# Kernel tuning notes

Measured on AMD Instinct MI355X. Metric: run time of the kernel, lower is better.

## Reference

```python
import jax, jax.numpy as jnp
import numpy as np

B, N, D = 2048, 65536, 128  # batch queries, max_engrams, spike_dim


def setup_inputs() -> dict:
    key = jax.random.key(0)
    k1, k2, k3, k4 = jax.random.split(key, 4)
    sensor_spikes = jax.random.normal(k1, (B, D), dtype=jnp.float32)
    # crystallize_skill stores sign(pattern), so keys/values are +-1 vectors
    sensor_keys = jnp.sign(jax.random.normal(k2, (N, D), dtype=jnp.float32))
    action_values = jnp.sign(jax.random.normal(k3, (N, D), dtype=jnp.float32))
    is_active = jax.random.bernoulli(k4, 0.5, (N,))
    return {
        "sensor_spikes": sensor_spikes,
        "sensor_keys": sensor_keys,
        "action_values": action_values,
        "is_active": is_active,
    }


def reference(sensor_spikes, sensor_keys, action_values, is_active):
    # similarity = x @ keys.T  -> [B, N]
    sim = jnp.einsum("bd,nd->bn", sensor_spikes.astype(jnp.float32), sensor_keys)
    # masked_fill_(~is_active, -inf)
    sim = jnp.where(is_active[None, :], sim, -jnp.inf)
    best_match_idx = jnp.argmax(sim, axis=-1)          # [B]
    confidence = jnp.max(sim, axis=-1)                 # [B] == sim[b, best_idx[b]]
    retrieved = action_values[best_match_idx]          # [B, D]
    return retrieved, confidence, best_match_idx
```

## Files before the change

### kernel.cpp

```cpp
#include <hip/hip_runtime.h>
#include <stdint.h>

typedef __attribute__((ext_vector_type(8))) short short8;
typedef __attribute__((ext_vector_type(4))) float f32x4;

#define NEG_INF (-__builtin_inff())

#define B_ROWS 2048
#define N_KEYS 65536
#define DIM    128


__device__ __forceinline__ unsigned short f2bf(float f) {
  unsigned u = __float_as_uint(f);
  u = (u + 0x7FFFu + ((u >> 16) & 1u)) >> 16;
  return (unsigned short)u;
}


__global__ __launch_bounds__(256) void convert_x_kernel(
    const float* __restrict__ x, short8* __restrict__ xi) {
  int t = blockIdx.x * 256 + threadIdx.x;
  int tile = t >> 11, loc = t & 2047;
  int rl = ((loc >> 8) << 4) + (loc & 15);
  int c = (loc >> 4) & 15;
  const float* src = x + (size_t)(tile * 128 + rl) * DIM + c * 8;
  f32x4 v0 = *(const f32x4*)(src);
  f32x4 v1 = *(const f32x4*)(src + 4);
  short8 o;
  o[0] = (short)f2bf(v0[0]); o[1] = (short)f2bf(v0[1]);
  o[2] = (short)f2bf(v0[2]); o[3] = (short)f2bf(v0[3]);
  o[4] = (short)f2bf(v1[0]); o[5] = (short)f2bf(v1[1]);
  o[6] = (short)f2bf(v1[2]); o[7] = (short)f2bf(v1[3]);
  xi[t] = o;
}

__global__ __launch_bounds__(256, 2) void sim3_kernel(
    const short8* __restrict__ xi, const float* __restrict__ keys,
    const int* __restrict__ act, float* __restrict__ cmax) {
  __shared__ short8 Bs[2048];
  const int tid = threadIdx.x;
  const int w = tid >> 6, l = tid & 63;
  const int ntile = blockIdx.x;

  const float* kb = keys + (size_t)ntile * (128 * DIM);
#pragma unroll
  for (int it = 0; it < 8; ++it) {
    int li = it * 256 + tid;
    int rl = ((li >> 8) << 4) + (li & 15);
    int c = (li >> 4) & 15;
    const float* src = kb + rl * DIM + c * 8;
    f32x4 v0 = *(const f32x4*)(src);
    f32x4 v1 = *(const f32x4*)(src + 4);
    int a = act[ntile * 128 + rl];
    short8 o;
    o[0] = (short)f2bf(v0[0]); o[1] = (short)f2bf(v0[1]);
    o[2] = (short)f2bf(v0[2]); o[3] = (short)f2bf(v0[3]);
    o[4] = (short)f2bf(v1[0]); o[5] = (short)f2bf(v1[1]);
    o[6] = (short)f2bf(v1[2]); o[7] = (short)f2bf(v1[3]);
    if (!a) o = short8{0, 0, 0, 0, 0, 0, 0, 0};
    Bs[li] = o;
  }
  __syncthreads();

  const int wr = w >> 1, wc = w & 1;
  const int lg = l >> 4, lr = l & 15;

  short8 bfv[4][4];
#pragma unroll
  for (int ni = 0; ni < 4; ni++)
#pragma unroll
    for (int kk = 0; kk < 4; kk++)
      bfv[ni][kk] = Bs[(wc * 4 + ni) * 256 + kk * 64 + l];

  const int chunk = ntile * 2 + wc;
  const short8* ag0 = xi + (wr * 4) * 256 + l;

  for (int bt = 0; bt < 16; ++bt) {
    short8 af[4][4];
#pragma unroll
    for (int mi = 0; mi < 4; mi++)
#pragma unroll
      for (int kk = 0; kk < 4; kk++)
        af[mi][kk] = ag0[(size_t)bt * 2048 + mi * 256 + kk * 64];

    f32x4 acc[4][4];
#pragma unroll
    for (int mi = 0; mi < 4; mi++)
#pragma unroll
      for (int ni = 0; ni < 4; ni++) acc[mi][ni] = f32x4{0.f, 0.f, 0.f, 0.f};

#pragma unroll
    for (int kk = 0; kk < 4; kk++)
#pragma unroll
      for (int mi = 0; mi < 4; mi++)
#pragma unroll
        for (int ni = 0; ni < 4; ni++)
          acc[mi][ni] = __builtin_amdgcn_mfma_f32_16x16x32_bf16(
              af[mi][kk], bfv[ni][kk], acc[mi][ni], 0, 0, 0);

#pragma unroll
    for (int mi = 0; mi < 4; mi++) {
      float rm[4];
#pragma unroll
      for (int r = 0; r < 4; r++)
        rm[r] = fmaxf(fmaxf(acc[mi][0][r], acc[mi][1][r]),
                      fmaxf(acc[mi][2][r], acc[mi][3][r]));
#pragma unroll
      for (int r = 0; r < 4; r++) {
        float v = rm[r];
        v = fmaxf(v, __shfl_xor(v, 1));
        v = fmaxf(v, __shfl_xor(v, 2));
        v = fmaxf(v, __shfl_xor(v, 4));
        v = fmaxf(v, __shfl_xor(v, 8));
        rm[r] = v;
      }
      if (lr == 0) {
        int row = bt * 128 + wr * 64 + mi * 16 + lg * 4;
#pragma unroll
        for (int r = 0; r < 4; r++)
          cmax[(size_t)(row + r) * 1024 + chunk] = rm[r];
      }
    }
  }
}

__global__ __launch_bounds__(256) void finalize_kernel(
    const float* __restrict__ x, const float* __restrict__ keys,
    const float* __restrict__ vals, const int* __restrict__ act,
    const float* __restrict__ cmax, float* __restrict__ out) {
  __shared__ float xr[128];
  __shared__ float wred[4];
  __shared__ int cand[96];
  __shared__ int ncand;
  __shared__ int bestn_s;
  __shared__ float skeys[64 * 129];
  const int b = blockIdx.x, tid = threadIdx.x;
  if (tid < 128) xr[tid] = x[(size_t)b * 128 + tid];
  if (tid == 0) ncand = 0;
  __syncthreads();

  const float* cm = cmax + (size_t)b * 1024;
  float c0 = cm[tid], c1 = cm[tid + 256], c2 = cm[tid + 512], c3 = cm[tid + 768];
  float lm = fmaxf(fmaxf(c0, c1), fmaxf(c2, c3));
#pragma unroll
  for (int s = 1; s < 64; s <<= 1) lm = fmaxf(lm, __shfl_xor(lm, s));
  if ((tid & 63) == 0) wred[tid >> 6] = lm;
  __syncthreads();
  float M = fmaxf(fmaxf(wred[0], wred[1]), fmaxf(wred[2], wred[3]));
  float thr = M - 0.75f;

  if (c0 > thr) { int p = atomicAdd(&ncand, 1); if (p < 96) cand[p] = tid; }
  if (c1 > thr) { int p = atomicAdd(&ncand, 1); if (p < 96) cand[p] = tid + 256; }
  if (c2 > thr) { int p = atomicAdd(&ncand, 1); if (p < 96) cand[p] = tid + 512; }
  if (c3 > thr) { int p = atomicAdd(&ncand, 1); if (p < 96) cand[p] = tid + 768; }
  __syncthreads();
  int nc = ncand; if (nc > 96) nc = 96;

  double bv = -(double)__builtin_inf();
  int bn = 0x7FFFFFFF;
  for (int ci = 0; ci < nc; ci++) {
    int cch = cand[ci];
    const float* kbase = keys + (size_t)cch * 64 * 128;
#pragma unroll
    for (int i = 0; i < 32; i++) {
      int idx = tid + i * 256;
      skeys[(idx >> 7) * 129 + (idx & 127)] = kbase[idx];
    }
    __syncthreads();
    if (tid < 64) {
      int n = cch * 64 + tid;
      if (act[n] != 0) {
        const float* kr = skeys + tid * 129;
        double s0 = 0.0, s1 = 0.0, s2 = 0.0, s3 = 0.0;
#pragma unroll
        for (int d = 0; d < 128; d += 4) {
          s0 += (double)xr[d] * (double)kr[d];
          s1 += (double)xr[d + 1] * (double)kr[d + 1];
          s2 += (double)xr[d + 2] * (double)kr[d + 2];
          s3 += (double)xr[d + 3] * (double)kr[d + 3];
        }
        double s = (s0 + s1) + (s2 + s3);
        if (s > bv || (s == bv && n < bn)) { bv = s; bn = n; }
      }
    }
    __syncthreads();
  }

  if (tid < 64) {
#pragma unroll
    for (int s = 1; s < 64; s <<= 1) {
      double ov = __shfl_xor(bv, s);
      int on = __shfl_xor(bn, s);
      if (ov > bv || (ov == bv && on < bn)) { bv = ov; bn = on; }
    }
    if (tid == 0) {
      bestn_s = bn;
      out[262144 + b] = (float)bv;
      out[264192 + b] = (float)bn;
    }
  }
  __syncthreads();
  int n = bestn_s;
  if (tid < 128) out[(size_t)b * 128 + tid] = vals[(size_t)n * 128 + tid];
}

__global__ __launch_bounds__(256) void direct_kernel(
    const float* __restrict__ x, const float* __restrict__ keys,
    const float* __restrict__ vals, const int* __restrict__ act,
    float* __restrict__ out) {
  __shared__ float xr[8][128];
  __shared__ double redv[8][4];
  __shared__ int redn[8][4];
  __shared__ int bests[8];
  const int tid = threadIdx.x;
  const int r0 = blockIdx.x * 8;
  const int w = tid >> 6, l = tid & 63;
#pragma unroll
  for (int i = 0; i < 4; i++) {
    int idx = tid + i * 256;
    xr[idx >> 7][idx & 127] = x[(size_t)(r0 + (idx >> 7)) * 128 + (idx & 127)];
  }
  __syncthreads();

  double bv[8];
  int bn[8];
#pragma unroll
  for (int r = 0; r < 8; r++) { bv[r] = -(double)__builtin_inf(); bn[r] = 0x7FFFFFFF; }

  for (int n = tid; n < N_KEYS; n += 256) {
    if (act[n] == 0) continue;
    const float* kr = keys + (size_t)n * 128;
    double s[8];
#pragma unroll
    for (int r = 0; r < 8; r++) s[r] = 0.0;
    for (int d = 0; d < 128; d += 4) {
      f32x4 kv = *(const f32x4*)(kr + d);
#pragma unroll
      for (int r = 0; r < 8; r++) {
        s[r] += (double)xr[r][d] * (double)kv[0];
        s[r] += (double)xr[r][d + 1] * (double)kv[1];
        s[r] += (double)xr[r][d + 2] * (double)kv[2];
        s[r] += (double)xr[r][d + 3] * (double)kv[3];
      }
    }
#pragma unroll
    for (int r = 0; r < 8; r++)
      if (s[r] > bv[r]) { bv[r] = s[r]; bn[r] = n; }
  }

#pragma unroll
  for (int r = 0; r < 8; r++) {
    double v = bv[r]; int n = bn[r];
#pragma unroll
    for (int s = 1; s < 64; s <<= 1) {
      double ov = __shfl_xor(v, s);
      int on = __shfl_xor(n, s);
      if (ov > v || (ov == v && on < n)) { v = ov; n = on; }
    }
    if (l == 0) { redv[r][w] = v; redn[r][w] = n; }
  }
  __syncthreads();
  if (tid < 8) {
    double v = redv[tid][0]; int n = redn[tid][0];
#pragma unroll
    for (int j = 1; j < 4; j++) {
      double ov = redv[tid][j]; int on = redn[tid][j];
      if (ov > v || (ov == v && on < n)) { v = ov; n = on; }
    }
    bests[tid] = n;
    out[262144 + r0 + tid] = (float)v;
    out[264192 + r0 + tid] = (float)n;
  }
  __syncthreads();
#pragma unroll
  for (int i = 0; i < 4; i++) {
    int idx = tid + i * 256;
    int r = idx >> 7, d = idx & 127;
    out[(size_t)(r0 + r) * 128 + d] = vals[(size_t)bests[r] * 128 + d];
  }
}

extern "C" void kernel_launch(void* const* d_in, const int* in_sizes, int n_in,
                              void* d_out, int out_size, void* d_ws, size_t ws_size,
                              hipStream_t stream) {
  const float* x    = (const float*)d_in[0];
  const float* keys = (const float*)d_in[1];
  const float* vals = (const float*)d_in[2];
  const int*   act  = (const int*)d_in[3];
  float* out = (float*)d_out;

  const size_t need = (size_t)16 * 2048 * sizeof(short8) +
                      (size_t)B_ROWS * 1024 * sizeof(float);
  if (ws_size >= need) {
    short8* xi   = (short8*)d_ws;
    float*  cmax = (float*)(xi + 16 * 2048);
    convert_x_kernel<<<128, 256, 0, stream>>>(x, xi);
    sim3_kernel<<<512, 256, 0, stream>>>(xi, keys, act, cmax);
    finalize_kernel<<<2048, 256, 0, stream>>>(x, keys, vals, act, cmax, out);
  } else {
    direct_kernel<<<256, 256, 0, stream>>>(x, keys, vals, act, out);
  }
}
```

Measured before the change: 178.2 us.

## Shrink per-wave MFMA tile to 32 keys and rework finalize rescoring

The similarity kernel now has each wave own 32 keys and stream 32 query rows per iteration, computing a 2x2 MFMA tile with operands swapped. The per-chunk maximum is then reduced across lane groups instead of within rows. This produces 2048 chunk maxima per query and raises the occupancy hint from 2 to 4 blocks. The finalize kernel drops the shared-memory key staging and rescoring loop: all 256 threads rescore each 32-key candidate chunk directly from global memory, 8 threads per key, combined by shuffles. The tradeoff is twice as much cmax traffic in exchange for smaller register tiles, higher occupancy and cheaper exact rescoring.

```diff
diff --git a/kernel.cpp b/kernel.cpp
--- a/kernel.cpp
+++ b/kernel.cpp
@@ -9,6 +9,7 @@
 #define B_ROWS 2048
 #define N_KEYS 65536
 #define DIM    128
+#define NCHUNK 2048
 
 
 __device__ __forceinline__ unsigned short f2bf(float f) {
@@ -21,10 +22,10 @@
 __global__ __launch_bounds__(256) void convert_x_kernel(
     const float* __restrict__ x, short8* __restrict__ xi) {
   int t = blockIdx.x * 256 + threadIdx.x;
-  int tile = t >> 11, loc = t & 2047;
-  int rl = ((loc >> 8) << 4) + (loc & 15);
-  int c = (loc >> 4) & 15;
-  const float* src = x + (size_t)(tile * 128 + rl) * DIM + c * 8;
+  int rb = t >> 8, loc = t & 255;
+  int rl = rb * 16 + (loc & 15);
+  int c = loc >> 4;
+  const float* src = x + (size_t)rl * DIM + c * 8;
   f32x4 v0 = *(const f32x4*)(src);
   f32x4 v1 = *(const f32x4*)(src + 4);
   short8 o;
@@ -35,7 +36,7 @@
   xi[t] = o;
 }
 
-__global__ __launch_bounds__(256, 2) void sim3_kernel(
+__global__ __launch_bounds__(256, 4) void sim4_kernel(
     const short8* __restrict__ xi, const float* __restrict__ keys,
     const int* __restrict__ act, float* __restrict__ cmax) {
   __shared__ short8 Bs[2048];
@@ -63,142 +64,138 @@
   }
   __syncthreads();
 
-  const int wr = w >> 1, wc = w & 1;
-  const int lg = l >> 4, lr = l & 15;
-
-  short8 bfv[4][4];
-#pragma unroll
-  for (int ni = 0; ni < 4; ni++)
+  short8 kf[2][4];
+#pragma unroll
+  for (int mi = 0; mi < 2; mi++)
 #pragma unroll
     for (int kk = 0; kk < 4; kk++)
-      bfv[ni][kk] = Bs[(wc * 4 + ni) * 256 + kk * 64 + l];
-
-  const int chunk = ntile * 2 + wc;
-  const short8* ag0 = xi + (wr * 4) * 256 + l;
-
-  for (int bt = 0; bt < 16; ++bt) {
-    short8 af[4][4];
-#pragma unroll
-    for (int mi = 0; mi < 4; mi++)
+      kf[mi][kk] = Bs[(w * 2 + mi) * 256 + kk * 64 + l];
+
+  const int chunk = ntile * 4 + w;
+  const int lr = l & 15;
+  float* cbase = cmax + chunk;
+
+  for (int it = 0; it < 64; ++it) {
+    short8 xf[2][4];
+#pragma unroll
+    for (int ni = 0; ni < 2; ni++)
 #pragma unroll
       for (int kk = 0; kk < 4; kk++)
-        af[mi][kk] = ag0[(size_t)bt * 2048 + mi * 256 + kk * 64];
-
-    f32x4 acc[4][4];
-#pragma unroll
-    for (int mi = 0; mi < 4; mi++)
-#pragma unroll
-      for (int ni = 0; ni < 4; ni++) acc[mi][ni] = f32x4{0.f, 0.f, 0.f, 0.f};
+        xf[ni][kk] = xi[(it * 2 + ni) * 256 + kk * 64 + l];
+
+    f32x4 acc[2][2];
+#pragma unroll
+    for (int mi = 0; mi < 2; mi++)
+#pragma unroll
+      for (int ni = 0; ni < 2; ni++) acc[mi][ni] = f32x4{0.f, 0.f, 0.f, 0.f};
 
 #pragma unroll
     for (int kk = 0; kk < 4; kk++)
 #pragma unroll
-      for (int mi = 0; mi < 4; mi++)
-#pragma unroll
-        for (int ni = 0; ni < 4; ni++)
+      for (int mi = 0; mi < 2; mi++)
+#pragma unroll
+        for (int ni = 0; ni < 2; ni++)
           acc[mi][ni] = __builtin_amdgcn_mfma_f32_16x16x32_bf16(
-              af[mi][kk], bfv[ni][kk], acc[mi][ni], 0, 0, 0);
-
-#pragma unroll
-    for (int mi = 0; mi < 4; mi++) {
-      float rm[4];
-#pragma unroll
-      for (int r = 0; r < 4; r++)
-        rm[r] = fmaxf(fmaxf(acc[mi][0][r], acc[mi][1][r]),
-                      fmaxf(acc[mi][2][r], acc[mi][3][r]));
-#pragma unroll
-      for (int r = 0; r < 4; r++) {
-        float v = rm[r];
-        v = fmaxf(v, __shfl_xor(v, 1));
-        v = fmaxf(v, __shfl_xor(v, 2));
-        v = fmaxf(v, __shfl_xor(v, 4));
-        v = fmaxf(v, __shfl_xor(v, 8));
-        rm[r] = v;
-      }
-      if (lr == 0) {
-        int row = bt * 128 + wr * 64 + mi * 16 + lg * 4;
-#pragma unroll
-        for (int r = 0; r < 4; r++)
-          cmax[(size_t)(row + r) * 1024 + chunk] = rm[r];
-      }
-    }
-  }
-}
-
-__global__ __launch_bounds__(256) void finalize_kernel(
+              kf[mi][kk], xf[ni][kk], acc[mi][ni], 0, 0, 0);
+
+#pragma unroll
+    for (int ni = 0; ni < 2; ni++) {
+      float t0 = fmaxf(acc[0][ni][0], acc[1][ni][0]);
+      float t1 = fmaxf(acc[0][ni][1], acc[1][ni][1]);
+      float t2 = fmaxf(acc[0][ni][2], acc[1][ni][2]);
+      float t3 = fmaxf(acc[0][ni][3], acc[1][ni][3]);
+      float v = fmaxf(fmaxf(t0, t1), fmaxf(t2, t3));
+      v = fmaxf(v, __shfl_xor(v, 16));
+      v = fmaxf(v, __shfl_xor(v, 32));
+      if (l < 16)
+        cbase[(size_t)(it * 32 + ni * 16 + lr) * NCHUNK] = v;
+    }
+  }
+}
+
+__global__ __launch_bounds__(256) void finalize2_kernel(
     const float* __restrict__ x, const float* __restrict__ keys,
     const float* __restrict__ vals, const int* __restrict__ act,
     const float* __restrict__ cmax, float* __restrict__ out) {
   __shared__ float xr[128];
   __shared__ float wred[4];
-  __shared__ int cand[96];
+  __shared__ int cand[256];
   __shared__ int ncand;
+  __shared__ double redv[4];
+  __shared__ int redn[4];
   __shared__ int bestn_s;
-  __shared__ float skeys[64 * 129];
   const int b = blockIdx.x, tid = threadIdx.x;
+  const int w = tid >> 6, l = tid & 63;
   if (tid < 128) xr[tid] = x[(size_t)b * 128 + tid];
   if (tid == 0) ncand = 0;
   __syncthreads();
 
-  const float* cm = cmax + (size_t)b * 1024;
-  float c0 = cm[tid], c1 = cm[tid + 256], c2 = cm[tid + 512], c3 = cm[tid + 768];
-  float lm = fmaxf(fmaxf(c0, c1), fmaxf(c2, c3));
+  const float* cm = cmax + (size_t)b * NCHUNK;
+  float c[8];
+  float lm = NEG_INF;
+#pragma unroll
+  for (int j = 0; j < 8; j++) {
+    c[j] = cm[tid + j * 256];
+    lm = fmaxf(lm, c[j]);
+  }
 #pragma unroll
   for (int s = 1; s < 64; s <<= 1) lm = fmaxf(lm, __shfl_xor(lm, s));
-  if ((tid & 63) == 0) wred[tid >> 6] = lm;
+  if (l == 0) wred[w] = lm;
   __syncthreads();
   float M = fmaxf(fmaxf(wred[0], wred[1]), fmaxf(wred[2], wred[3]));
   float thr = M - 0.75f;
 
-  if (c0 > thr) { int p = atomicAdd(&ncand, 1); if (p < 96) cand[p] = tid; }
-  if (c1 > thr) { int p = atomicAdd(&ncand, 1); if (p < 96) cand[p] = tid + 256; }
-  if (c2 > thr) { int p = atomicAdd(&ncand, 1); if (p < 96) cand[p] = tid + 512; }
-  if (c3 > thr) { int p = atomicAdd(&ncand, 1); if (p < 96) cand[p] = tid + 768; }
-  __syncthreads();
-  int nc = ncand; if (nc > 96) nc = 96;
+#pragma unroll
+  for (int j = 0; j < 8; j++) {
+    if (c[j] > thr) {
+      int p = atomicAdd(&ncand, 1);
+      if (p < 256) cand[p] = tid + j * 256;
+    }
+  }
+  __syncthreads();
+  int nc = ncand; if (nc > 256) nc = 256;
 
   double bv = -(double)__builtin_inf();
   int bn = 0x7FFFFFFF;
+  const int key_off = tid >> 3;
+  const int d0 = (tid & 7) * 16;
   for (int ci = 0; ci < nc; ci++) {
-    int cch = cand[ci];
-    const float* kbase = keys + (size_t)cch * 64 * 128;
-#pragma unroll
-    for (int i = 0; i < 32; i++) {
-      int idx = tid + i * 256;
-      skeys[(idx >> 7) * 129 + (idx & 127)] = kbase[idx];
-    }
-    __syncthreads();
-    if (tid < 64) {
-      int n = cch * 64 + tid;
-      if (act[n] != 0) {
-        const float* kr = skeys + tid * 129;
-        double s0 = 0.0, s1 = 0.0, s2 = 0.0, s3 = 0.0;
-#pragma unroll
-        for (int d = 0; d < 128; d += 4) {
-          s0 += (double)xr[d] * (double)kr[d];
-          s1 += (double)xr[d + 1] * (double)kr[d + 1];
-          s2 += (double)xr[d + 2] * (double)kr[d + 2];
-          s3 += (double)xr[d + 3] * (double)kr[d + 3];
-        }
-        double s = (s0 + s1) + (s2 + s3);
-        if (s > bv || (s == bv && n < bn)) { bv = s; bn = n; }
-      }
-    }
-    __syncthreads();
-  }
-
-  if (tid < 64) {
-#pragma unroll
-    for (int s = 1; s < 64; s <<= 1) {
-      double ov = __shfl_xor(bv, s);
-      int on = __shfl_xor(bn, s);
-      if (ov > bv || (ov == bv && on < bn)) { bv = ov; bn = on; }
-    }
-    if (tid == 0) {
-      bestn_s = bn;
-      out[262144 + b] = (float)bv;
-      out[264192 + b] = (float)bn;
-    }
+    int n = cand[ci] * 32 + key_off;
+    const float* kr = keys + (size_t)n * 128 + d0;
+    double s = 0.0;
+#pragma unroll
+    for (int u = 0; u < 16; u += 4) {
+      f32x4 kv = *(const f32x4*)(kr + u);
+      s += (double)xr[d0 + u] * (double)kv[0];
+      s += (double)xr[d0 + u + 1] * (double)kv[1];
+      s += (double)xr[d0 + u + 2] * (double)kv[2];
+      s += (double)xr[d0 + u + 3] * (double)kv[3];
+    }
+    s += __shfl_xor(s, 1);
+    s += __shfl_xor(s, 2);
+    s += __shfl_xor(s, 4);
+    if ((tid & 7) == 0 && act[n] != 0) {
+      if (s > bv || (s == bv && n < bn)) { bv = s; bn = n; }
+    }
+  }
+
+#pragma unroll
+  for (int s = 1; s < 64; s <<= 1) {
+    double ov = __shfl_xor(bv, s);
+    int on = __shfl_xor(bn, s);
+    if (ov > bv || (ov == bv && on < bn)) { bv = ov; bn = on; }
+  }
+  if (l == 0) { redv[w] = bv; redn[w] = bn; }
+  __syncthreads();
+  if (tid == 0) {
+    double v = redv[0]; int n = redn[0];
+#pragma unroll
+    for (int j = 1; j < 4; j++) {
+      if (redv[j] > v || (redv[j] == v && redn[j] < n)) { v = redv[j]; n = redn[j]; }
+    }
+    bestn_s = n;
+    out[262144 + b] = (float)v;
+    out[264192 + b] = (float)n;
   }
   __syncthreads();
   int n = bestn_s;
@@ -290,14 +287,14 @@
   const int*   act  = (const int*)d_in[3];
   float* out = (float*)d_out;
 
-  const size_t need = (size_t)16 * 2048 * sizeof(short8) +
-                      (size_t)B_ROWS * 1024 * sizeof(float);
+  const size_t need = (size_t)32768 * sizeof(short8) +
+                      (size_t)B_ROWS * NCHUNK * sizeof(float);
   if (ws_size >= need) {
     short8* xi   = (short8*)d_ws;
-    float*  cmax = (float*)(xi + 16 * 2048);
+    float*  cmax = (float*)(xi + 32768);
     convert_x_kernel<<<128, 256, 0, stream>>>(x, xi);
-    sim3_kernel<<<512, 256, 0, stream>>>(xi, keys, act, cmax);
-    finalize_kernel<<<2048, 256, 0, stream>>>(x, keys, vals, act, cmax, out);
+    sim4_kernel<<<512, 256, 0, stream>>>(xi, keys, act, cmax);
+    finalize2_kernel<<<2048, 256, 0, stream>>>(x, keys, vals, act, cmax, out);
   } else {
     direct_kernel<<<256, 256, 0, stream>>>(x, keys, vals, act, out);
   }
```

Result: no change. 176.3 us (-1.0%).
